# Kernel optimization log

Hardware: AMD Instinct MI355X
Metric: run time of the kernel (lower is better)

Reference implementation:

```python
import jax, jax.numpy as jnp
import numpy as np

B, T, D, H = 4, 4096, 1024, 16
HD = D // H

def _phi(x):
    # ELU + 1 feature map (positive values)
    return jax.nn.elu(x) + 1.0

def setup_inputs() -> dict:
    key = jax.random.key(0)
    ks = jax.random.split(key, 6)
    s = D ** -0.5
    return {
        "x": jax.random.normal(ks[0], (B, T, D), dtype=jnp.float32),
        "mask": jax.random.randint(ks[1], (B, 1, 1, T), 0, 2).astype(bool),
        "Wq": jax.random.normal(ks[2], (D, D), dtype=jnp.float32) * s,
        "Wk": jax.random.normal(ks[3], (D, D), dtype=jnp.float32) * s,
        "Wv": jax.random.normal(ks[4], (D, D), dtype=jnp.float32) * s,
        "Wo": jax.random.normal(ks[5], (D, D), dtype=jnp.float32) * s,
    }

def reference(x, mask, Wq, Wk, Wv, Wo):
    b, t, d = x.shape
    def proj(W):
        # nn.Linear: y = x @ W.T ; split heads -> (B, H, T, HD)
        return (x @ W.T).reshape(b, t, H, HD).transpose(0, 2, 1, 3)
    q = _phi(proj(Wq))
    k = _phi(proj(Wk))
    v = proj(Wv)
    # mask.transpose(-2,-1): (B,1,1,T) -> (B,1,T,1); True positions zeroed
    m = jnp.swapaxes(mask, -2, -1)
    k = jnp.where(m, 0.0, k)
    v = jnp.where(m, 0.0, v)
    # kv = k^T v : (B,H,HD,HD) global pooling over T
    kv = jnp.einsum('bhtd,bhte->bhde', k, v)
    k_sum = k.sum(axis=-2)  # (B,H,HD)
    out = jnp.einsum('bhtd,bhde->bhte', q, kv)  # (B,H,T,HD)
    norm = jnp.maximum(jnp.einsum('bhtd,bhd->bht', q, k_sum)[..., None], 1e-6)
    out = (out / norm).transpose(0, 2, 1, 3).reshape(b, t, d)
    return out @ Wo.T  # dropout=0 (eval) -> identity
```

## Files before the change

### kernel.cpp

```cpp
#include <hip/hip_runtime.h>
#include <hip/hip_bf16.h>
#include <stdint.h>

#define T_ 4096
#define M_ 16384

typedef __attribute__((ext_vector_type(8))) short short8;
typedef __attribute__((ext_vector_type(4))) float f32x4;

__device__ __forceinline__ short f2b(float f) {
    __hip_bfloat16 h = __float2bfloat16(f);
    return __builtin_bit_cast(short, h);
}
__device__ __forceinline__ float b2f(short s) {
    unsigned int u = ((unsigned int)(unsigned short)s) << 16;
    return __builtin_bit_cast(float, u);
}
__device__ __forceinline__ void gload16(const void* g, void* l) {
    __builtin_amdgcn_global_load_lds(
        (const __attribute__((address_space(1))) void*)(unsigned long long)(uintptr_t)g,
        (__attribute__((address_space(3))) void*)(unsigned int)(uintptr_t)l,
        16, 0, 0);
}

__global__ __launch_bounds__(256) void cvt_x(const float* __restrict__ in,
                                             short* __restrict__ out) {
    long i = ((long)blockIdx.x * 256 + threadIdx.x) * 4;
    float4 f = *(const float4*)(in + i);
    short4 o; o.x = f2b(f.x); o.y = f2b(f.y); o.z = f2b(f.z); o.w = f2b(f.w);
    *(short4*)(out + i) = o;
}

__global__ __launch_bounds__(256) void cvt_weights(
    const float* __restrict__ Wq, const float* __restrict__ Wk,
    const float* __restrict__ Wv, const float* __restrict__ Wo,
    short* __restrict__ wqkvb, short* __restrict__ wob) {
    long i = ((long)blockIdx.x * 256 + threadIdx.x) * 4;
    int region = (int)(i >> 20);
    long off = i & 1048575;
    const float* src = region == 0 ? Wq : region == 1 ? Wk : region == 2 ? Wv : Wo;
    short* dst = region < 3 ? wqkvb + (long)region * 1048576 : wob;
    float4 f = *(const float4*)(src + off);
    short4 o; o.x = f2b(f.x); o.y = f2b(f.y); o.z = f2b(f.z); o.w = f2b(f.w);
    *(short4*)(dst + off) = o;
}

template <int MODE>
__global__ __launch_bounds__(512) void gemm4s(
    const short* __restrict__ A, const short* __restrict__ Bw,
    const int* __restrict__ mask,
    short* __restrict__ oQ, short* __restrict__ oK, short* __restrict__ oV,
    float* __restrict__ oF) {
    extern __shared__ short lds[];
    const int tid = threadIdx.x;
    const int wave = tid >> 6, lane = tid & 63;
    const int wm = wave >> 2, wn = wave & 3;

    const int nwg = gridDim.x;
    const int cpx = nwg >> 3;
    const int wg = (blockIdx.x & 7) * cpx + (blockIdx.x >> 3);
    const int NB = (MODE == 0) ? 12 : 4;
    const int bn = wg % NB, bm = wg / NB;
    const long m0 = (long)bm * 256, n0 = (long)bn * 256;

    f32x4 acc[8][4];
#pragma unroll
    for (int i = 0; i < 8; ++i)
#pragma unroll
        for (int j = 0; j < 4; ++j) acc[i][j] = (f32x4)(0.0f);

    const short* aStageBase = A + (m0 + (lane >> 3)) * 1024 +
                              (((lane & 7) ^ (lane >> 3)) * 8);
    const short* bStageBase = Bw + (n0 + (lane >> 3)) * 1024 +
                              (((lane & 7) ^ (lane >> 3)) * 8);

    auto stageA = [&](int t) {
        const int d = t & 1;
#pragma unroll
        for (int j = 0; j < 4; ++j) {
            const int r = wave * 8 + j * 64;
            gload16(aStageBase + (long)r * 1024 + t * 64, lds + d * 16384 + r * 64);
        }
    };
    auto stageB = [&](int t) {
        const int d = t & 1;
#pragma unroll
        for (int j = 0; j < 4; ++j) {
            const int r = wave * 8 + j * 64;
            gload16(bStageBase + (long)r * 1024 + t * 64,
                    lds + 32768 + d * 16384 + r * 64);
        }
    };

    const int laneR = lane & 15;
    const int sB0 = (((lane >> 4) ^ (lane & 7)) * 8);
    const int cA0 = wm * 8192 + laneR * 64 + sB0;
    const int cA1 = wm * 8192 + laneR * 64 + (sB0 ^ 32);
    const int cB0 = 32768 + (wn >> 1) * 8192 + (wn & 1) * 4096 +
                    laneR * 64 + sB0;
    const int cB1 = 32768 + (wn >> 1) * 8192 + (wn & 1) * 4096 +
                    laneR * 64 + (sB0 ^ 32);

    short8 alo[4][2], ahi[4][2], blo[2][2], bhi[2][2];
    auto rdAlo = [&](int pa0, int pa1) {
#pragma unroll
        for (int m = 0; m < 4; ++m) {
            alo[m][0] = *(const short8*)(lds + pa0 + m * 1024);
            alo[m][1] = *(const short8*)(lds + pa1 + m * 1024);
        }
    };
    auto rdAhi = [&](int pa0, int pa1) {
#pragma unroll
        for (int m = 0; m < 4; ++m) {
            ahi[m][0] = *(const short8*)(lds + pa0 + 4096 + m * 1024);
            ahi[m][1] = *(const short8*)(lds + pa1 + 4096 + m * 1024);
        }
    };
    auto rdBlo = [&](int pb0, int pb1) {
#pragma unroll
        for (int n = 0; n < 2; ++n) {
            blo[n][0] = *(const short8*)(lds + pb0 + n * 1024);
            blo[n][1] = *(const short8*)(lds + pb1 + n * 1024);
        }
    };
    auto rdBhi = [&](int pb0, int pb1) {
#pragma unroll
        for (int n = 0; n < 2; ++n) {
            bhi[n][0] = *(const short8*)(lds + pb0 + 2048 + n * 1024);
            bhi[n][1] = *(const short8*)(lds + pb1 + 2048 + n * 1024);
        }
    };
    auto mm = [&](short8 (&a)[4][2], short8 (&b)[2][2], int mo, int no) {
        __builtin_amdgcn_s_setprio(1);
#pragma unroll
        for (int kk = 0; kk < 2; ++kk)
#pragma unroll
            for (int m = 0; m < 4; ++m)
#pragma unroll
                for (int n = 0; n < 2; ++n)
                    acc[mo + m][no + n] = __builtin_amdgcn_mfma_f32_16x16x32_bf16(
                        a[m][kk], b[n][kk], acc[mo + m][no + n], 0, 0, 0);
        __builtin_amdgcn_s_setprio(0);
    };

#define BAR()    __builtin_amdgcn_s_barrier()
#define LGKM0()  asm volatile("s_waitcnt lgkmcnt(0)" ::: "memory")
#define VMW0()   asm volatile("s_waitcnt vmcnt(0)" ::: "memory")
#define SCHED0() __builtin_amdgcn_sched_barrier(0)

    stageA(0); stageB(0);
    VMW0();
    BAR();
    SCHED0();

#pragma unroll 2
    for (int t = 0; t < 16; ++t) {
        const int dofs = (t & 1) * 16384;
        const int pa0 = cA0 + dofs, pa1 = cA1 + dofs;
        const int pb0 = cB0 + dofs, pb1 = cB1 + dofs;
        if (t + 1 < 16) stageA(t + 1);
        rdAlo(pa0, pa1); rdBlo(pb0, pb1);
        BAR(); LGKM0(); SCHED0();
        mm(alo, blo, 0, 0);
        BAR();
        if (t + 1 < 16) stageB(t + 1);
        rdAhi(pa0, pa1);
        BAR(); LGKM0(); SCHED0();
        mm(ahi, blo, 4, 0);
        BAR();
        rdBhi(pb0, pb1);
        BAR(); LGKM0(); SCHED0();
        mm(ahi, bhi, 4, 2);
        BAR();
        mm(alo, bhi, 0, 2);
        VMW0();
        BAR(); SCHED0();
    }

    if (MODE == 0) {
        const int sec = (int)(n0 >> 10);
        short* outp = sec == 0 ? oQ : (sec == 1 ? oK : oV);
        const long cbase = n0 & 1023;
#pragma unroll
        for (int mi = 0; mi < 8; ++mi) {
#pragma unroll
            for (int r = 0; r < 4; ++r) {
                long gm = m0 + wm * 128 + mi * 16 + (lane >> 4) * 4 + r;
                int mz = (sec >= 1) ? mask[gm] : 0;
#pragma unroll
                for (int ni = 0; ni < 4; ++ni) {
                    long gn = cbase + wn * 64 + ni * 16 + (lane & 15);
                    float v = acc[mi][ni][r];
                    if (sec <= 1) v = (v > 0.f) ? v + 1.f : __expf(v);
                    if (mz) v = 0.f;
                    outp[gm * 1024 + gn] = f2b(v);
                }
            }
        }
    } else {
#pragma unroll
        for (int mi = 0; mi < 8; ++mi)
#pragma unroll
            for (int r = 0; r < 4; ++r) {
                long gm = m0 + wm * 128 + mi * 16 + (lane >> 4) * 4 + r;
#pragma unroll
                for (int ni = 0; ni < 4; ++ni) {
                    long gn = n0 + wn * 64 + ni * 16 + (lane & 15);
                    oF[gm * 1024 + gn] = acc[mi][ni][r];
                }
            }
    }
#undef BAR
#undef LGKM0
#undef VMW0
#undef SCHED0
}

__global__ __launch_bounds__(256) void kv_partial(
    const short* __restrict__ Kb, const short* __restrict__ Vb,
    float* __restrict__ kvp, float* __restrict__ ksp) {
    __shared__ __align__(16) float Ks[64][64];
    __shared__ __align__(16) float Vs[64][64];
    const int c = blockIdx.x, bh = blockIdx.y;
    const int b = bh >> 4, h = bh & 15;
    const int tid = threadIdx.x;
    const int dk = tid & 63, g = tid >> 6;
    float acc[16];
#pragma unroll
    for (int j = 0; j < 16; ++j) acc[j] = 0.f;
    float ks = 0.f;
    const long rowbase = (long)b * T_ + (long)c * 256;
    const int col0 = h * 64;

    for (int s = 0; s < 4; ++s) {
        __syncthreads();
        {
            int rr = tid >> 2;
            int cc = (tid & 3) * 16;
            const long gr = rowbase + s * 64 + rr;
            const short* kp = Kb + gr * 1024 + col0 + cc;
            const short* vp = Vb + gr * 1024 + col0 + cc;
            short8 k0 = *(const short8*)(kp);
            short8 k1 = *(const short8*)(kp + 8);
            short8 v0 = *(const short8*)(vp);
            short8 v1 = *(const short8*)(vp + 8);
            float kf[16], vf[16];
#pragma unroll
            for (int e = 0; e < 8; ++e) {
                kf[e] = b2f(k0[e]); kf[8 + e] = b2f(k1[e]);
                vf[e] = b2f(v0[e]); vf[8 + e] = b2f(v1[e]);
            }
#pragma unroll
            for (int q = 0; q < 4; ++q) {
                *(f32x4*)&Ks[rr][cc + q * 4] = *(f32x4*)&kf[q * 4];
                *(f32x4*)&Vs[rr][cc + q * 4] = *(f32x4*)&vf[q * 4];
            }
        }
        __syncthreads();
#pragma unroll 8
        for (int tt = 0; tt < 64; ++tt) {
            float kv_ = Ks[tt][dk];
            if (g == 0) ks += kv_;
            f32x4 v0 = *(const f32x4*)&Vs[tt][g * 16];
            f32x4 v1 = *(const f32x4*)&Vs[tt][g * 16 + 4];
            f32x4 v2 = *(const f32x4*)&Vs[tt][g * 16 + 8];
            f32x4 v3 = *(const f32x4*)&Vs[tt][g * 16 + 12];
#pragma unroll
            for (int e = 0; e < 4; ++e) {
                acc[e] += kv_ * v0[e];  acc[4 + e] += kv_ * v1[e];
                acc[8 + e] += kv_ * v2[e]; acc[12 + e] += kv_ * v3[e];
            }
        }
    }
    float* dst = kvp + ((long)bh * 16 + c) * 4096 + dk * 64 + g * 16;
#pragma unroll
    for (int q = 0; q < 4; ++q) *(f32x4*)(dst + q * 4) = *(f32x4*)&acc[q * 4];
    if (g == 0) ksp[((long)bh * 16 + c) * 64 + dk] = ks;
}

__global__ __launch_bounds__(256) void kv_reduce(
    const float* __restrict__ kvp, const float* __restrict__ ksp,
    short* __restrict__ kvT) {
    const int bh = blockIdx.x;
    const int tid = threadIdx.x;
    for (int e = tid; e < 4096; e += 256) {
        int dk = e >> 6, dv = e & 63;
        float s = 0.f;
#pragma unroll
        for (int c = 0; c < 16; ++c) s += kvp[((long)bh * 16 + c) * 4096 + e];
        kvT[(long)bh * 5120 + dv * 64 + dk] = f2b(s);
    }
    if (tid < 64) {
        float s = 0.f;
#pragma unroll
        for (int c = 0; c < 16; ++c) s += ksp[((long)bh * 16 + c) * 64 + tid];
        kvT[(long)bh * 5120 + 64 * 64 + tid] = f2b(s);
    }
    for (int e = tid; e < 15 * 64; e += 256)
        kvT[(long)bh * 5120 + 65 * 64 + e] = 0;
}

__global__ __launch_bounds__(256) void attn_out(
    const short* __restrict__ Qb, const short* __restrict__ kvT,
    short* __restrict__ attn) {
    __shared__ __align__(16) short Qs[128 * 64];
    const int tb = blockIdx.x, bh = blockIdx.y;
    const int b = bh >> 4, h = bh & 15;
    const int tid = threadIdx.x, wave = tid >> 6, lane = tid & 63;
    const long trow0 = (long)b * T_ + (long)tb * 128;
    const int col0 = h * 64;

    const int lr = lane >> 3, lc = (lane & 7) * 8;
    const short* qsrc = Qb + (trow0 + wave * 8 + lr) * 1024 + col0 + lc;
#pragma unroll
    for (int is = 0; is < 4; ++is)
        gload16(qsrc + (long)is * 32 * 1024, Qs + is * 2048 + wave * 512);

    short8 bfr[5][2];
    const short* kvb = kvT + (long)bh * 5120;
#pragma unroll
    for (int nf = 0; nf < 5; ++nf)
#pragma unroll
        for (int kk = 0; kk < 2; ++kk)
            bfr[nf][kk] = *(const short8*)(kvb + (nf * 16 + (lane & 15)) * 64 +
                                           kk * 32 + (lane >> 4) * 8);
    __syncthreads();

#pragma unroll
    for (int tf = 0; tf < 2; ++tf) {
        short8 af[2];
        int ar = wave * 32 + tf * 16 + (lane & 15);
#pragma unroll
        for (int kk = 0; kk < 2; ++kk)
            af[kk] = *(const short8*)(Qs + ar * 64 + kk * 32 + (lane >> 4) * 8);
        f32x4 oacc[5];
#pragma unroll
        for (int nf = 0; nf < 5; ++nf) {
            oacc[nf] = (f32x4)(0.0f);
#pragma unroll
            for (int kk = 0; kk < 2; ++kk)
                oacc[nf] = __builtin_amdgcn_mfma_f32_16x16x32_bf16(
                    af[kk], bfr[nf][kk], oacc[nf], 0, 0, 0);
        }
#pragma unroll
        for (int r = 0; r < 4; ++r) {
            float nv = __shfl(oacc[4][r], lane & 48, 64);
            nv = fmaxf(nv, 1e-6f);
            long gm = trow0 + wave * 32 + tf * 16 + (lane >> 4) * 4 + r;
#pragma unroll
            for (int nf = 0; nf < 4; ++nf) {
                float v = oacc[nf][r] / nv;
                attn[gm * 1024 + col0 + nf * 16 + (lane & 15)] = f2b(v);
            }
        }
    }
}

extern "C" void kernel_launch(void* const* d_in, const int* in_sizes, int n_in,
                              void* d_out, int out_size, void* d_ws, size_t ws_size,
                              hipStream_t stream) {
    const float* x = (const float*)d_in[0];
    const int* mask = (const int*)d_in[1];
    const float* Wq = (const float*)d_in[2];
    const float* Wk = (const float*)d_in[3];
    const float* Wv = (const float*)d_in[4];
    const float* Wo = (const float*)d_in[5];
    float* out = (float*)d_out;
    char* ws = (char*)d_ws;

    short* xb    = (short*)(ws);
    short* wqkvb = (short*)(ws + 33554432);
    short* wob   = (short*)(ws + 39845888);
    short* Qb    = (short*)(ws + 41943040);
    short* Kb    = (short*)(ws + 75497472);
    short* Vb    = (short*)(ws + 109051904);
    float* kvp   = (float*)(ws + 142606336);
    float* ksp   = (float*)(ws + 159383552);
    short* kvT   = (short*)(ws + 159645696);
    short* attnb = xb;

    hipFuncSetAttribute((const void*)gemm4s<0>,
                        hipFuncAttributeMaxDynamicSharedMemorySize, 131072);
    hipFuncSetAttribute((const void*)gemm4s<1>,
                        hipFuncAttributeMaxDynamicSharedMemorySize, 131072);

    cvt_x<<<16384, 256, 0, stream>>>(x, xb);
    cvt_weights<<<4096, 256, 0, stream>>>(Wq, Wk, Wv, Wo, wqkvb, wob);
    gemm4s<0><<<768, 512, 131072, stream>>>(xb, wqkvb, mask, Qb, Kb, Vb, nullptr);
    kv_partial<<<dim3(16, 64), 256, 0, stream>>>(Kb, Vb, kvp, ksp);
    kv_reduce<<<64, 256, 0, stream>>>(kvp, ksp, kvT);
    attn_out<<<dim3(32, 64), 256, 0, stream>>>(Qb, kvT, attnb);
    gemm4s<1><<<256, 512, 131072, stream>>>(attnb, wob, nullptr, nullptr, nullptr,
                                            nullptr, out);
}
```

Before: 250.1 us.

## Compute KV outer-product partials with bf16 MFMA and merge conversion kernels

Replaces the scalar fp32 FMA loop in the per-chunk K^T V accumulation with bf16 MFMA 16x16x32. K and V are staged transposed into swizzled LDS so each wave can read MFMA operands along T, and the K column sums come from a separate LDS reduction. The x and weight bf16 conversion kernels are also fused into one launch to save a launch. The KV partials are still accumulated in fp32, and the transposed LDS scatter stores may cause bank conflicts.

New measurement: 225.6 us. 1.11x faster.

```diff
diff --git a/kernel.cpp b/kernel.cpp
--- a/kernel.cpp
+++ b/kernel.cpp
@@ -23,26 +23,27 @@
         16, 0, 0);
 }
 
-__global__ __launch_bounds__(256) void cvt_x(const float* __restrict__ in,
-                                             short* __restrict__ out) {
-    long i = ((long)blockIdx.x * 256 + threadIdx.x) * 4;
-    float4 f = *(const float4*)(in + i);
-    short4 o; o.x = f2b(f.x); o.y = f2b(f.y); o.z = f2b(f.z); o.w = f2b(f.w);
-    *(short4*)(out + i) = o;
-}
-
-__global__ __launch_bounds__(256) void cvt_weights(
+__global__ __launch_bounds__(256) void cvt_all(
+    const float* __restrict__ x,
     const float* __restrict__ Wq, const float* __restrict__ Wk,
     const float* __restrict__ Wv, const float* __restrict__ Wo,
-    short* __restrict__ wqkvb, short* __restrict__ wob) {
-    long i = ((long)blockIdx.x * 256 + threadIdx.x) * 4;
-    int region = (int)(i >> 20);
-    long off = i & 1048575;
-    const float* src = region == 0 ? Wq : region == 1 ? Wk : region == 2 ? Wv : Wo;
-    short* dst = region < 3 ? wqkvb + (long)region * 1048576 : wob;
-    float4 f = *(const float4*)(src + off);
-    short4 o; o.x = f2b(f.x); o.y = f2b(f.y); o.z = f2b(f.z); o.w = f2b(f.w);
-    *(short4*)(dst + off) = o;
+    short* __restrict__ xb, short* __restrict__ wqkvb, short* __restrict__ wob) {
+    if (blockIdx.x < 16384) {
+        long i = ((long)blockIdx.x * 256 + threadIdx.x) * 4;
+        float4 f = *(const float4*)(x + i);
+        short4 o; o.x = f2b(f.x); o.y = f2b(f.y); o.z = f2b(f.z); o.w = f2b(f.w);
+        *(short4*)(xb + i) = o;
+    } else {
+        long i = ((long)(blockIdx.x - 16384) * 256 + threadIdx.x) * 4;
+        int region = (int)(i >> 20);
+        long off = i & 1048575;
+        const float* src = region == 0 ? Wq : region == 1 ? Wk
+                                            : region == 2 ? Wv : Wo;
+        short* dst = region < 3 ? wqkvb + (long)region * 1048576 : wob;
+        float4 f = *(const float4*)(src + off);
+        short4 o; o.x = f2b(f.x); o.y = f2b(f.y); o.z = f2b(f.z); o.w = f2b(f.w);
+        *(short4*)(dst + off) = o;
+    }
 }
 
 template <int MODE>
@@ -216,66 +217,79 @@
 #undef SCHED0
 }
 
-__global__ __launch_bounds__(256) void kv_partial(
+__global__ __launch_bounds__(256) void kv_mfma(
     const short* __restrict__ Kb, const short* __restrict__ Vb,
     float* __restrict__ kvp, float* __restrict__ ksp) {
-    __shared__ __align__(16) float Ks[64][64];
-    __shared__ __align__(16) float Vs[64][64];
+    __shared__ __align__(16) short Kt[64 * 256];
+    __shared__ __align__(16) short Vt[64 * 256];
+    __shared__ float ksred[256];
     const int c = blockIdx.x, bh = blockIdx.y;
     const int b = bh >> 4, h = bh & 15;
-    const int tid = threadIdx.x;
-    const int dk = tid & 63, g = tid >> 6;
-    float acc[16];
-#pragma unroll
-    for (int j = 0; j < 16; ++j) acc[j] = 0.f;
-    float ks = 0.f;
+    const int tid = threadIdx.x, wave = tid >> 6, lane = tid & 63;
     const long rowbase = (long)b * T_ + (long)c * 256;
     const int col0 = h * 64;
 
-    for (int s = 0; s < 4; ++s) {
-        __syncthreads();
+    for (int e = 0; e < 8; ++e) {
+        int chunk = tid + e * 256;
+        int trow = chunk >> 3;
+        int c8 = (chunk & 7) * 8;
+        short8 kv8 = *(const short8*)(Kb + (rowbase + trow) * 1024 + col0 + c8);
+        short8 vv8 = *(const short8*)(Vb + (rowbase + trow) * 1024 + col0 + c8);
+#pragma unroll
+        for (int j = 0; j < 8; ++j) {
+            int col = c8 + j;
+            int tp = (trow & 7) | ((((trow >> 3) ^ (col & 7)) & 31) << 3);
+            Kt[col * 256 + tp] = kv8[j];
+            Vt[col * 256 + tp] = vv8[j];
+        }
+    }
+    __syncthreads();
+
+    const int lr = lane & 15, lk = lane >> 4;
+    f32x4 acc[4];
+#pragma unroll
+    for (int m = 0; m < 4; ++m) acc[m] = (f32x4)(0.0f);
+    for (int ts = 0; ts < 8; ++ts) {
+        short8 bf;
         {
-            int rr = tid >> 2;
-            int cc = (tid & 3) * 16;
-            const long gr = rowbase + s * 64 + rr;
-            const short* kp = Kb + gr * 1024 + col0 + cc;
-            const short* vp = Vb + gr * 1024 + col0 + cc;
-            short8 k0 = *(const short8*)(kp);
-            short8 k1 = *(const short8*)(kp + 8);
-            short8 v0 = *(const short8*)(vp);
-            short8 v1 = *(const short8*)(vp + 8);
-            float kf[16], vf[16];
-#pragma unroll
-            for (int e = 0; e < 8; ++e) {
-                kf[e] = b2f(k0[e]); kf[8 + e] = b2f(k1[e]);
-                vf[e] = b2f(v0[e]); vf[8 + e] = b2f(v1[e]);
-            }
-#pragma unroll
-            for (int q = 0; q < 4; ++q) {
-                *(f32x4*)&Ks[rr][cc + q * 4] = *(f32x4*)&kf[q * 4];
-                *(f32x4*)&Vs[rr][cc + q * 4] = *(f32x4*)&vf[q * 4];
-            }
-        }
-        __syncthreads();
-#pragma unroll 8
-        for (int tt = 0; tt < 64; ++tt) {
-            float kv_ = Ks[tt][dk];
-            if (g == 0) ks += kv_;
-            f32x4 v0 = *(const f32x4*)&Vs[tt][g * 16];
-            f32x4 v1 = *(const f32x4*)&Vs[tt][g * 16 + 4];
-            f32x4 v2 = *(const f32x4*)&Vs[tt][g * 16 + 8];
-            f32x4 v3 = *(const f32x4*)&Vs[tt][g * 16 + 12];
-#pragma unroll
-            for (int e = 0; e < 4; ++e) {
-                acc[e] += kv_ * v0[e];  acc[4 + e] += kv_ * v1[e];
-                acc[8 + e] += kv_ * v2[e]; acc[12 + e] += kv_ * v3[e];
-            }
-        }
-    }
-    float* dst = kvp + ((long)bh * 16 + c) * 4096 + dk * 64 + g * 16;
-#pragma unroll
-    for (int q = 0; q < 4; ++q) *(f32x4*)(dst + q * 4) = *(f32x4*)&acc[q * 4];
-    if (g == 0) ksp[((long)bh * 16 + c) * 64 + dk] = ks;
+            int row = wave * 16 + lr;
+            int slot = ((ts * 4 + lk) ^ (row & 7)) & 31;
+            bf = *(const short8*)(Vt + row * 256 + slot * 8);
+        }
+#pragma unroll
+        for (int m = 0; m < 4; ++m) {
+            int row = m * 16 + lr;
+            int slot = ((ts * 4 + lk) ^ (row & 7)) & 31;
+            short8 af = *(const short8*)(Kt + row * 256 + slot * 8);
+            acc[m] = __builtin_amdgcn_mfma_f32_16x16x32_bf16(af, bf, acc[m], 0, 0, 0);
+        }
+    }
+
+    {
+        int dk = tid & 63, q = tid >> 6;
+        float s = 0.f;
+#pragma unroll
+        for (int j = 0; j < 8; ++j) {
+            short8 v = *(const short8*)(Kt + dk * 256 + q * 64 + j * 8);
+#pragma unroll
+            for (int e2 = 0; e2 < 8; ++e2) s += b2f(v[e2]);
+        }
+        ksred[tid] = s;
+    }
+    __syncthreads();
+
+    float* dst = kvp + ((long)bh * 16 + c) * 4096;
+#pragma unroll
+    for (int m = 0; m < 4; ++m)
+#pragma unroll
+        for (int r = 0; r < 4; ++r) {
+            int dk = m * 16 + lk * 4 + r;
+            dst[dk * 64 + wave * 16 + lr] = acc[m][r];
+        }
+    if (tid < 64) {
+        float s = ksred[tid] + ksred[tid + 64] + ksred[tid + 128] + ksred[tid + 192];
+        ksp[((long)bh * 16 + c) * 64 + tid] = s;
+    }
 }
 
 __global__ __launch_bounds__(256) void kv_reduce(
@@ -384,10 +398,9 @@
     hipFuncSetAttribute((const void*)gemm4s<1>,
                         hipFuncAttributeMaxDynamicSharedMemorySize, 131072);
 
-    cvt_x<<<16384, 256, 0, stream>>>(x, xb);
-    cvt_weights<<<4096, 256, 0, stream>>>(Wq, Wk, Wv, Wo, wqkvb, wob);
+    cvt_all<<<20480, 256, 0, stream>>>(x, Wq, Wk, Wv, Wo, xb, wqkvb, wob);
     gemm4s<0><<<768, 512, 131072, stream>>>(xb, wqkvb, mask, Qb, Kb, Vb, nullptr);
-    kv_partial<<<dim3(16, 64), 256, 0, stream>>>(Kb, Vb, kvp, ksp);
+    kv_mfma<<<dim3(16, 64), 256, 0, stream>>>(Kb, Vb, kvp, ksp);
     kv_reduce<<<64, 256, 0, stream>>>(kvp, ksp, kvT);
     attn_out<<<dim3(32, 64), 256, 0, stream>>>(Qb, kvT, attnb);
     gemm4s<1><<<256, 512, 131072, stream>>>(attnb, wob, nullptr, nullptr, nullptr,
```
